# Kernel optimization log

Hardware: AMD Instinct MI355X
Metric: run time of the kernel (lower is better)

## Reference

```python
import jax, jax.numpy as jnp
import numpy as np

N = 100000      # nodes
E = 1600000     # directed edges (avg degree 16)
D_IN = 64
D_OUT = 64


def setup_inputs() -> dict:
    key = jax.random.key(0)
    k1, k2, k3, k4, k5 = jax.random.split(key, 5)
    x = jax.random.normal(k1, (N, D_IN), dtype=jnp.float32)
    edge_index = jax.random.randint(k2, (2, E), 0, N, dtype=jnp.int32)
    s_in = 1.0 / np.sqrt(D_IN)
    W_conv = jax.random.normal(k3, (D_IN, D_OUT), dtype=jnp.float32) * s_in
    b_conv = jnp.zeros((D_OUT,), dtype=jnp.float32)
    W_self = jax.random.normal(k4, (D_IN, D_OUT), dtype=jnp.float32) * s_in
    b_self = jax.random.normal(k5, (D_OUT,), dtype=jnp.float32) * s_in
    return {"x": x, "edge_index": edge_index, "W_conv": W_conv, "b_conv": b_conv,
            "W_self": W_self, "b_self": b_self, "n1": 400, "n2": 250}


def reference(x, edge_index, W_conv, b_conv, W_self, b_self, n1, n2):
    # GCNConv (PyG defaults): add self-loops, symmetric normalization,
    # out_i = sum_j norm_ij * (x_j @ W_conv) + b_conv; then self-loop linear + residual.
    n = x.shape[0]
    loops = jnp.arange(n, dtype=edge_index.dtype)
    row = jnp.concatenate([edge_index[0], loops])  # source nodes [E+N]
    col = jnp.concatenate([edge_index[1], loops])  # target nodes [E+N]
    deg = jax.ops.segment_sum(jnp.ones_like(col, dtype=x.dtype), col, num_segments=n)
    dinv = jnp.where(deg > 0, jax.lax.rsqrt(deg), 0.0)      # deg^{-1/2}
    norm = dinv[row] * dinv[col]                            # [E+N]
    xw = x @ W_conv                                         # [N, D_OUT]
    msg = xw[row] * norm[:, None]                           # gather + scale [E+N, D_OUT]
    x_neigh = jax.ops.segment_sum(msg, col, num_segments=n) + b_conv
    x_self = x @ W_self + b_self
    return x_self + x_neigh
```

## Files before the change

kernel.cpp:

```cpp
#include <hip/hip_runtime.h>

#define CAP 64
#define CHUNK 8192
#define NBINS_MAX 1024
#define CAPB 2560

typedef __attribute__((ext_vector_type(8))) short bf16x8;
typedef __attribute__((ext_vector_type(4))) float f32x4;

__device__ __forceinline__ unsigned short f2bf_rne(float f) {
    unsigned u = __builtin_bit_cast(unsigned, f);
    u += 0x7FFFu + ((u >> 16) & 1u);
    return (unsigned short)(u >> 16);
}
__device__ __forceinline__ float bf2f(unsigned short h) {
    return __builtin_bit_cast(float, (unsigned)h << 16);
}


__global__ void k_zero(int* __restrict__ gcur, int nbins, int* __restrict__ degovf,
                       int n, int* __restrict__ ovfc) {
    int i = blockIdx.x * blockDim.x + threadIdx.x;
    if (i < nbins) gcur[i] = 0;
    if (i < n) degovf[i] = 0;
    if (i == 0) *ovfc = 0;
}

__global__ void k_wprep(const float* __restrict__ Wc, const float* __restrict__ Ws,
                        unsigned short* __restrict__ bfrag) {
    const int t = threadIdx.x;
    for (int s = t; s < 2048; s += 256) {
        int lane = s & 63;
        int ct   = (s >> 6) & 3;
        int ks   = (s >> 8) & 1;
        int half = (s >> 9) & 1;
        int mat  = (s >> 10) & 1;
        const float* W = mat ? Ws : Wc;
        int d = ct * 16 + (lane & 15);
        int kbase = ks * 32 + (lane >> 4) * 8;
#pragma unroll
        for (int j = 0; j < 8; ++j) {
            float v = W[(kbase + j) * 64 + d];
            unsigned u = __builtin_bit_cast(unsigned, v);
            unsigned short hi = (unsigned short)(u >> 16);
            unsigned short elem;
            if (half == 0) {
                elem = hi;
            } else {
                float fh = __builtin_bit_cast(float, (unsigned)hi << 16);
                float fl = v - fh;
                elem = (unsigned short)(__builtin_bit_cast(unsigned, fl) >> 16);
            }
            bfrag[(size_t)s * 8 + j] = elem;
        }
    }
}

__global__ __launch_bounds__(512) void k_bin(
    const int* __restrict__ row, const int* __restrict__ col, int e, int nbins,
    int* __restrict__ gcur, unsigned int* __restrict__ records,
    int* __restrict__ degovf, int* __restrict__ ovf, int* __restrict__ ovfc)
{
    __shared__ int hist[NBINS_MAX];
    __shared__ int lofs[NBINS_MAX];
    __shared__ int gadj[NBINS_MAX];
    __shared__ int tscan[512];
    __shared__ unsigned int stage[CHUNK];
    __shared__ unsigned short sbin[CHUNK];

    const int t = threadIdx.x;
    const int base = blockIdx.x * CHUNK;
    int cnt = e - base; if (cnt > CHUNK) cnt = CHUNK;
    if (cnt <= 0) return;

    for (int i = t; i < nbins; i += 512) hist[i] = 0;
    __syncthreads();

    for (int k = t; k < cnt; k += 512) atomicAdd(&hist[col[base + k] >> 7], 1);
    __syncthreads();

    const int b0 = t * 2;
    int h0 = (b0 < nbins) ? hist[b0] : 0;
    int h1 = (b0 + 1 < nbins) ? hist[b0 + 1] : 0;
    int s = h0 + h1;
    tscan[t] = s;
    __syncthreads();
    for (int off = 1; off < 512; off <<= 1) {
        int v = (t >= off) ? tscan[t - off] : 0;
        __syncthreads();
        tscan[t] += v;
        __syncthreads();
    }
    const int tbase = tscan[t] - s;

    if (b0 < nbins) {
        int gb = h0 ? atomicAdd(&gcur[b0], h0) : 0;
        lofs[b0] = tbase; gadj[b0] = gb - tbase;
    }
    if (b0 + 1 < nbins) {
        int lb = tbase + h0;
        int gb = h1 ? atomicAdd(&gcur[b0 + 1], h1) : 0;
        lofs[b0 + 1] = lb; gadj[b0 + 1] = gb - lb;
    }
    __syncthreads();

    for (int k = t; k < cnt; k += 512) {
        int c = col[base + k];
        int r = row[base + k];
        int b = c >> 7;
        int slot = atomicAdd(&lofs[b], 1);
        stage[slot] = ((unsigned)r << 7) | (unsigned)(c & 127);
        sbin[slot] = (unsigned short)b;
    }
    __syncthreads();

    for (int k = t; k < cnt; k += 512) {
        unsigned rec = stage[k];
        int b = sbin[k];
        int g = gadj[b] + k;
        if (g < CAPB) {
            records[(size_t)b * CAPB + g] = rec;
        } else {
            int q = atomicAdd(ovfc, 1);
            int c = (b << 7) | (int)(rec & 127u);
            ovf[2 * q]     = (int)(rec >> 7);
            ovf[2 * q + 1] = c;
            atomicAdd(&degovf[c], 1);
        }
    }
}

__global__ __launch_bounds__(256) void k_dinv(
    const int* __restrict__ gcur, const unsigned int* __restrict__ records,
    const int* __restrict__ degovf, float* __restrict__ dinv, int n)
{
    __shared__ int lh[128];
    const int b = blockIdx.x, t = threadIdx.x;
    if (t < 128) lh[t] = 0;
    __syncthreads();
    int m = gcur[b]; if (m > CAPB) m = CAPB;
    const unsigned int* rb = records + (size_t)b * CAPB;
    for (int k = t; k < m; k += 256) atomicAdd(&lh[rb[k] & 127u], 1);
    __syncthreads();
    if (t < 128) {
        int node = (b << 7) + t;
        if (node < n) dinv[node] = rsqrtf((float)(lh[t] + degovf[node] + 1));
    }
}

__global__ __launch_bounds__(256) void k_gemm5(
    const float* __restrict__ x, const unsigned short* __restrict__ bfrag,
    const float* __restrict__ bc, const float* __restrict__ bs,
    const float* __restrict__ dinv, unsigned short* __restrict__ ybf,
    float* __restrict__ out, int n)
{
    const int t = threadIdx.x;
    const int lane = t & 63;
    const int wid = t >> 6;
    const int rt0 = blockIdx.x * 128 + wid * 32;
    if (rt0 >= n) return;

    const int arow = lane & 15;
    const int kgrp = lane >> 4;

    bf16x8 a_hi[2][2], a_lo[2][2];
#pragma unroll
    for (int rt = 0; rt < 2; ++rt) {
        int row = rt0 + rt * 16 + arow;
        if (row >= n) row = n - 1;
        const float* xp = x + (size_t)row * 64 + kgrp * 8;
#pragma unroll
        for (int ks = 0; ks < 2; ++ks) {
            float4 f0 = *(const float4*)(xp + ks * 32);
            float4 f1 = *(const float4*)(xp + ks * 32 + 4);
            float f[8] = {f0.x, f0.y, f0.z, f0.w, f1.x, f1.y, f1.z, f1.w};
            bf16x8 h, l;
#pragma unroll
            for (int j = 0; j < 8; ++j) {
                unsigned u = __builtin_bit_cast(unsigned, f[j]);
                unsigned short hj = (unsigned short)(u >> 16);
                float fh = __builtin_bit_cast(float, (unsigned)hj << 16);
                float fl = f[j] - fh;
                unsigned short lj = (unsigned short)(__builtin_bit_cast(unsigned, fl) >> 16);
                h[j] = (short)hj;
                l[j] = (short)lj;
            }
            a_hi[rt][ks] = h;
            a_lo[rt][ks] = l;
        }
    }

    f32x4 acc[2][2][4];
#pragma unroll
    for (int m = 0; m < 2; ++m)
#pragma unroll
        for (int rt = 0; rt < 2; ++rt)
#pragma unroll
            for (int ct = 0; ct < 4; ++ct)
                acc[m][rt][ct] = (f32x4){0.f, 0.f, 0.f, 0.f};

#pragma unroll
    for (int mat = 0; mat < 2; ++mat) {
#pragma unroll
        for (int ks = 0; ks < 2; ++ks) {
#pragma unroll
            for (int ct = 0; ct < 4; ++ct) {
                const bf16x8 bh = *(const bf16x8*)(bfrag + ((size_t)((((mat * 2 + 0) * 2 + ks) * 4 + ct) * 64 + lane)) * 8);
                const bf16x8 bl = *(const bf16x8*)(bfrag + ((size_t)((((mat * 2 + 1) * 2 + ks) * 4 + ct) * 64 + lane)) * 8);
#pragma unroll
                for (int rt = 0; rt < 2; ++rt) {
                    acc[mat][rt][ct] = __builtin_amdgcn_mfma_f32_16x16x32_bf16(a_hi[rt][ks], bh, acc[mat][rt][ct], 0, 0, 0);
                    acc[mat][rt][ct] = __builtin_amdgcn_mfma_f32_16x16x32_bf16(a_lo[rt][ks], bh, acc[mat][rt][ct], 0, 0, 0);
                    acc[mat][rt][ct] = __builtin_amdgcn_mfma_f32_16x16x32_bf16(a_hi[rt][ks], bl, acc[mat][rt][ct], 0, 0, 0);
                }
            }
        }
    }

    const int dcol = lane & 15;
    const int rbase = (lane >> 4) * 4;
    float di[2][4];
#pragma unroll
    for (int rt = 0; rt < 2; ++rt)
#pragma unroll
        for (int reg = 0; reg < 4; ++reg) {
            int row = rt0 + rt * 16 + rbase + reg;
            di[rt][reg] = dinv[(row < n) ? row : (n - 1)];
        }

#pragma unroll
    for (int ct = 0; ct < 4; ++ct) {
        int d = ct * 16 + dcol;
        float bias = bc[d] + bs[d];
#pragma unroll
        for (int rt = 0; rt < 2; ++rt) {
#pragma unroll
            for (int reg = 0; reg < 4; ++reg) {
                int row = rt0 + rt * 16 + rbase + reg;
                if (row < n) {
                    float dv = di[rt][reg];
                    float zc = acc[0][rt][ct][reg];
                    ybf[(size_t)row * 64 + d] = f2bf_rne(zc * dv);
                    out[(size_t)row * 64 + d] = acc[1][rt][ct][reg] + bias + dv * dv * zc;
                }
            }
        }
    }
}

__global__ __launch_bounds__(512) void k_gather_bin2(
    const int* __restrict__ gcur, const unsigned int* __restrict__ records,
    const unsigned short* __restrict__ ybf, const float* __restrict__ dinv,
    float* __restrict__ out, int n)
{
    __shared__ unsigned int srec[CAPB];
    __shared__ int slist[CAPB];
    __shared__ int scnt[128];
    __shared__ int sinc[128];
    __shared__ int scur[128];

    const int b = blockIdx.x, t = threadIdx.x;
    int m = gcur[b]; if (m > CAPB) m = CAPB;

    if (t < 128) scnt[t] = 0;
    __syncthreads();

    for (int k = t; k < m; k += 512) {
        unsigned r = __builtin_nontemporal_load(&records[(size_t)b * CAPB + k]);
        srec[k] = r;
        atomicAdd(&scnt[r & 127u], 1);
    }
    __syncthreads();

    if (t < 128) sinc[t] = scnt[t];
    __syncthreads();
    for (int off = 1; off < 128; off <<= 1) {
        int v = 0;
        if (t < 128 && t >= off) v = sinc[t - off];
        __syncthreads();
        if (t < 128) sinc[t] += v;
        __syncthreads();
    }
    if (t < 128) scur[t] = sinc[t] - scnt[t];
    __syncthreads();

    for (int k = t; k < m; k += 512) {
        unsigned r = srec[k];
        int slot = atomicAdd(&scur[r & 127u], 1);
        slist[slot] = (int)(r >> 7);
    }
    __syncthreads();

    const int wave = t >> 6, lane = t & 63;
    for (int i = wave; i < 128; i += 8) {
        int node = (b << 7) + i;
        if (node >= n) break;
        int cnt = scnt[i];
        if (cnt == 0) continue;
        int beg = sinc[i] - cnt;
        float acc = 0.f;
        for (int base = 0; base < cnt; base += 64) {
            int mm = cnt - base; if (mm > 64) mm = 64;
            int rl = (lane < mm) ? slist[beg + base + lane] : 0;
            float a0=0.f,a1=0.f,a2=0.f,a3=0.f,a4=0.f,a5=0.f,a6=0.f,a7=0.f;
            int k = 0;
            for (; k + 8 <= mm; k += 8) {
                int r0=__shfl(rl,k+0), r1=__shfl(rl,k+1), r2=__shfl(rl,k+2), r3=__shfl(rl,k+3);
                int r4=__shfl(rl,k+4), r5=__shfl(rl,k+5), r6=__shfl(rl,k+6), r7=__shfl(rl,k+7);
                unsigned short v0 = ybf[(size_t)r0*64 + lane];
                unsigned short v1 = ybf[(size_t)r1*64 + lane];
                unsigned short v2 = ybf[(size_t)r2*64 + lane];
                unsigned short v3 = ybf[(size_t)r3*64 + lane];
                unsigned short v4 = ybf[(size_t)r4*64 + lane];
                unsigned short v5 = ybf[(size_t)r5*64 + lane];
                unsigned short v6 = ybf[(size_t)r6*64 + lane];
                unsigned short v7 = ybf[(size_t)r7*64 + lane];
                a0 += bf2f(v0); a1 += bf2f(v1); a2 += bf2f(v2); a3 += bf2f(v3);
                a4 += bf2f(v4); a5 += bf2f(v5); a6 += bf2f(v6); a7 += bf2f(v7);
            }
            for (; k + 2 <= mm; k += 2) {
                int r0=__shfl(rl,k+0), r1=__shfl(rl,k+1);
                a0 += bf2f(ybf[(size_t)r0*64 + lane]);
                a1 += bf2f(ybf[(size_t)r1*64 + lane]);
            }
            if (k < mm) { int r0=__shfl(rl,k); a0 += bf2f(ybf[(size_t)r0*64 + lane]); }
            acc += ((a0+a1)+(a2+a3)) + ((a4+a5)+(a6+a7));
        }
        float* op = out + (size_t)node*64 + lane;
        float prev = __builtin_nontemporal_load(op);
        __builtin_nontemporal_store(prev + dinv[node] * acc, op);
    }
}

__global__ void k_ovf2(const int* __restrict__ ovfc, const int* __restrict__ ovf,
                       const float* __restrict__ dinv, const unsigned short* __restrict__ ybf,
                       float* __restrict__ out) {
    int m = *ovfc;
    long long total = (long long)m * 64;
    for (long long idx = blockIdx.x * blockDim.x + threadIdx.x; idx < total;
         idx += (long long)gridDim.x * blockDim.x) {
        int q = (int)(idx >> 6);
        int j = (int)(idx & 63);
        int r = ovf[2 * q], c = ovf[2 * q + 1];
        float s = dinv[c];
        float v = bf2f(ybf[(size_t)r * 64 + j]);
        unsafeAtomicAdd(out + (size_t)c * 64 + j, s * v);
    }
}


__global__ void k_init(int* __restrict__ cnt, int* __restrict__ ovf_cnt, int n) {
    int i = blockIdx.x * blockDim.x + threadIdx.x;
    if (i < n) cnt[i] = 0;
    if (i == 0) *ovf_cnt = 0;
}

__global__ void k_fill_pad(const int* __restrict__ row, const int* __restrict__ col,
                           int* __restrict__ cnt, int* __restrict__ bucket,
                           int* __restrict__ ovf, int* __restrict__ ovf_cnt, int e) {
    int i = blockIdx.x * blockDim.x + threadIdx.x;
    if (i >= e) return;
    int c = col[i];
    int p = atomicAdd(&cnt[c], 1);
    if (p < CAP) bucket[(size_t)c * CAP + p] = row[i];
    else { int q = atomicAdd(ovf_cnt, 1); ovf[q] = i; }
}

__global__ __launch_bounds__(256) void k_gemm(
    const float* __restrict__ x, const float* __restrict__ Wc,
    const float* __restrict__ bc, const float* __restrict__ Ws,
    const float* __restrict__ bs, const int* __restrict__ deg, int add,
    float* __restrict__ dinv, float* __restrict__ y,
    float* __restrict__ out, int n)
{
    __shared__ __align__(16) float sWc[64 * 64];
    __shared__ __align__(16) float sWs[64 * 64];
    __shared__ __align__(16) float sx[64 * 64];
    const int t = threadIdx.x;

    for (int i = t; i < 1024; i += 256) {
        ((float4*)sWc)[i] = ((const float4*)Wc)[i];
        ((float4*)sWs)[i] = ((const float4*)Ws)[i];
    }
    const int row0 = blockIdx.x * 64;
    int nrows = n - row0; if (nrows > 64) nrows = 64;
    for (int i = t; i < nrows * 16; i += 256) {
        ((float4*)sx)[i] = ((const float4*)(x + (size_t)row0 * 64))[i];
    }
    __syncthreads();

    const int d = t & 63;
    const int g = t >> 6;

    float wcr[64], wsr[64];
#pragma unroll
    for (int k = 0; k < 64; ++k) { wcr[k] = sWc[k * 64 + d]; wsr[k] = sWs[k * 64 + d]; }

    const float bcd = bc[d], bsd = bs[d];

    for (int rr = g * 16; rr < (g + 1) * 16; ++rr) {
        if (rr >= nrows) break;
        float accC = 0.f, accS = 0.f;
        const float4* xv4 = (const float4*)(sx + rr * 64);
#pragma unroll
        for (int q = 0; q < 16; ++q) {
            float4 xv = xv4[q];
            accC += xv.x*wcr[4*q+0] + xv.y*wcr[4*q+1] + xv.z*wcr[4*q+2] + xv.w*wcr[4*q+3];
            accS += xv.x*wsr[4*q+0] + xv.y*wsr[4*q+1] + xv.z*wsr[4*q+2] + xv.w*wsr[4*q+3];
        }
        const int r = row0 + rr;
        const float di = rsqrtf((float)(deg[r] + add));
        if (d == 0) dinv[r] = di;
        const float yv = accC * di;
        y[(size_t)r * 64 + d] = yv;
        out[(size_t)r * 64 + d] = accS + bsd + bcd + di * yv;
    }
}

__global__ __launch_bounds__(256) void k_gather_pad(
    const int* __restrict__ cnt, const int* __restrict__ bucket,
    const float* __restrict__ y, float* __restrict__ out, int n)
{
    const int node = blockIdx.x * 4 + (threadIdx.x >> 6);
    if (node >= n) return;
    const int lane = threadIdx.x & 63;
    int m = cnt[node];
    const float di = rsqrtf((float)(m + 1));
    if (m > CAP) m = CAP;
    if (m == 0) return;

    int rl = (lane < m) ? bucket[(size_t)node * CAP + lane] : 0;

    float a0=0.f,a1=0.f,a2=0.f,a3=0.f,a4=0.f,a5=0.f,a6=0.f,a7=0.f;
    int k = 0;
    for (; k + 8 <= m; k += 8) {
        int r0=__shfl(rl,k+0), r1=__shfl(rl,k+1), r2=__shfl(rl,k+2), r3=__shfl(rl,k+3);
        int r4=__shfl(rl,k+4), r5=__shfl(rl,k+5), r6=__shfl(rl,k+6), r7=__shfl(rl,k+7);
        a0 += y[(size_t)r0*64 + lane];
        a1 += y[(size_t)r1*64 + lane];
        a2 += y[(size_t)r2*64 + lane];
        a3 += y[(size_t)r3*64 + lane];
        a4 += y[(size_t)r4*64 + lane];
        a5 += y[(size_t)r5*64 + lane];
        a6 += y[(size_t)r6*64 + lane];
        a7 += y[(size_t)r7*64 + lane];
    }
    for (; k + 2 <= m; k += 2) {
        int r0=__shfl(rl,k+0), r1=__shfl(rl,k+1);
        a0 += y[(size_t)r0*64 + lane];
        a1 += y[(size_t)r1*64 + lane];
    }
    if (k < m) { int r0=__shfl(rl,k); a0 += y[(size_t)r0*64 + lane]; }

    float acc = ((a0+a1)+(a2+a3)) + ((a4+a5)+(a6+a7));
    out[(size_t)node*64 + lane] += di * acc;
}

__global__ void k_ovf_idx(const int* __restrict__ ovf_cnt, const int* __restrict__ ovf,
                          const int* __restrict__ row, const int* __restrict__ col,
                          const float* __restrict__ dinv, const float* __restrict__ y,
                          float* __restrict__ out) {
    int m = *ovf_cnt;
    long long total = (long long)m * 16;
    for (long long idx = blockIdx.x*blockDim.x+threadIdx.x; idx < total;
         idx += (long long)gridDim.x*blockDim.x) {
        int ei = ovf[idx >> 4];
        int j = (int)(idx & 15);
        int r = row[ei], c = col[ei];
        float s = dinv[c];
        float4 v = ((const float4*)y)[(size_t)r*16 + j];
        float* o = out + (size_t)c*64 + (j<<2);
        unsafeAtomicAdd(o+0, s*v.x);
        unsafeAtomicAdd(o+1, s*v.y);
        unsafeAtomicAdd(o+2, s*v.z);
        unsafeAtomicAdd(o+3, s*v.w);
    }
}

__global__ void k_deg_init(int* __restrict__ deg, int n) {
    int i = blockIdx.x * blockDim.x + threadIdx.x;
    if (i < n) deg[i] = 1;
}

__global__ void k_deg_count(const int* __restrict__ col, int* __restrict__ deg, int e) {
    int i = blockIdx.x * blockDim.x + threadIdx.x;
    if (i < e) atomicAdd(&deg[col[i]], 1);
}

__global__ __launch_bounds__(256) void k_scatter(
    const int* __restrict__ row, const int* __restrict__ col,
    const float* __restrict__ dinv, const float* __restrict__ y,
    float* __restrict__ out, int e)
{
    int idx = blockIdx.x * blockDim.x + threadIdx.x;
    int eidx = idx >> 4;
    if (eidx >= e) return;
    int j = idx & 15;
    int r = row[eidx];
    int c = col[eidx];
    float s = dinv[c];
    float4 v = ((const float4*)y)[(size_t)r * 16 + j];
    float* o = out + (size_t)c * 64 + (j << 2);
    unsafeAtomicAdd(o + 0, s * v.x);
    unsafeAtomicAdd(o + 1, s * v.y);
    unsafeAtomicAdd(o + 2, s * v.z);
    unsafeAtomicAdd(o + 3, s * v.w);
}

extern "C" void kernel_launch(void* const* d_in, const int* in_sizes, int n_in,
                              void* d_out, int out_size, void* d_ws, size_t ws_size,
                              hipStream_t stream) {
    const float* x  = (const float*)d_in[0];
    const int*   ei = (const int*)d_in[1];
    const float* Wc = (const float*)d_in[2];
    const float* bc = (const float*)d_in[3];
    const float* Ws = (const float*)d_in[4];
    const float* bs = (const float*)d_in[5];
    float* out = (float*)d_out;

    const int n = in_sizes[0] / 64;
    const int e = in_sizes[1] / 2;
    const int* rowi = ei;
    const int* coli = ei + e;

    auto align = [](size_t v) { return (v + 255) & ~(size_t)255; };
    char* ws = (char*)d_ws;
    const int nbins = (n + 127) >> 7;

    size_t m_dinv = 0;
    size_t m_y    = align(m_dinv + (size_t)n * 4);
    size_t m_gcur = align(m_y    + (size_t)n * 128);
    size_t m_rec  = align(m_gcur + (size_t)nbins * 4);
    size_t m_dov  = align(m_rec  + (size_t)nbins * CAPB * 4);
    size_t m_ovf  = align(m_dov  + (size_t)n * 4);
    size_t m_ovfc = align(m_ovf  + (size_t)e * 8);
    size_t m_bfr  = align(m_ovfc + 256);
    size_t m_tot  = m_bfr + 32768;

    size_t p_cnt  = 0;
    size_t p_dinv = align(p_cnt  + (size_t)n * 4);
    size_t p_y    = align(p_dinv + (size_t)n * 4);
    size_t p_bkt  = align(p_y    + (size_t)n * 256);
    size_t p_ovf  = align(p_bkt  + (size_t)n * CAP * 4);
    size_t p_ovfc = align(p_ovf  + (size_t)e * 4);
    size_t p_tot  = p_ovfc + 256;

    if (nbins <= NBINS_MAX && m_tot <= ws_size) {
        float* dinv = (float*)(ws + m_dinv);
        unsigned short* ybf = (unsigned short*)(ws + m_y);
        int*   gcur = (int*)(ws + m_gcur);
        unsigned int* rec = (unsigned int*)(ws + m_rec);
        int*   dov  = (int*)(ws + m_dov);
        int*   ovf  = (int*)(ws + m_ovf);
        int*   ovfc = (int*)(ws + m_ovfc);
        unsigned short* bfrag = (unsigned short*)(ws + m_bfr);

        int zmax = (n > nbins) ? n : nbins;
        k_zero<<<(zmax + 255) / 256, 256, 0, stream>>>(gcur, nbins, dov, n, ovfc);
        k_wprep<<<1, 256, 0, stream>>>(Wc, Ws, bfrag);
        k_bin<<<(e + CHUNK - 1) / CHUNK, 512, 0, stream>>>(rowi, coli, e, nbins,
                                                           gcur, rec, dov, ovf, ovfc);
        k_dinv<<<nbins, 256, 0, stream>>>(gcur, rec, dov, dinv, n);
        k_gemm5<<<(n + 127) / 128, 256, 0, stream>>>(x, bfrag, bc, bs, dinv, ybf, out, n);
        k_gather_bin2<<<nbins, 512, 0, stream>>>(gcur, rec, ybf, dinv, out, n);
        k_ovf2<<<64, 256, 0, stream>>>(ovfc, ovf, dinv, ybf, out);
    } else if (p_tot <= ws_size) {
        int*   cnt    = (int*)(ws + p_cnt);
        float* dinv   = (float*)(ws + p_dinv);
        float* y      = (float*)(ws + p_y);
        int*   bucket = (int*)(ws + p_bkt);
        int*   ovf    = (int*)(ws + p_ovf);
        int*   ovfc   = (int*)(ws + p_ovfc);

        k_init<<<(n + 255) / 256, 256, 0, stream>>>(cnt, ovfc, n);
        k_fill_pad<<<(e + 255) / 256, 256, 0, stream>>>(rowi, coli, cnt, bucket, ovf, ovfc, e);
        k_gemm<<<(n + 63) / 64, 256, 0, stream>>>(x, Wc, bc, Ws, bs, cnt, 1, dinv, y, out, n);
        k_gather_pad<<<(n + 3) / 4, 256, 0, stream>>>(cnt, bucket, y, out, n);
        k_ovf_idx<<<64, 256, 0, stream>>>(ovfc, ovf, rowi, coli, dinv, y, out);
    } else {
        size_t a_deg  = 0;
        size_t a_dinv = align(a_deg  + (size_t)n * 4);
        size_t a_y    = align(a_dinv + (size_t)n * 4);
        int*   deg  = (int*)(ws + a_deg);
        float* dinv = (float*)(ws + a_dinv);
        float* y    = (float*)(ws + a_y);
        k_deg_init<<<(n + 255) / 256, 256, 0, stream>>>(deg, n);
        k_deg_count<<<(e + 255) / 256, 256, 0, stream>>>(coli, deg, e);
        k_gemm<<<(n + 63) / 64, 256, 0, stream>>>(x, Wc, bc, Ws, bs, deg, 0, dinv, y, out, n);
        long long tot = (long long)e * 16;
        k_scatter<<<(int)((tot + 255) / 256), 256, 0, stream>>>(rowi, coli, dinv, y, out, e);
    }
}
```

Baseline: 115.1 us.

## Split gather bins across two blocks and fuse weight prep into zero kernel

The gather kernel now launches two blocks per 128-node bin. Each block handles 64 destination nodes and filters the bin's records to its own half, which doubles block-level parallelism at the cost of each block reading all records of the bin. The weight-fragment preparation is merged into the zeroing kernel as an extra last block, removing one kernel launch. The gather change trades redundant record loading and LDS work for more concurrent blocks (782 to 1564).

```diff
diff --git a/kernel.cpp b/kernel.cpp
--- a/kernel.cpp
+++ b/kernel.cpp
@@ -18,42 +18,43 @@
 }
 
 
-__global__ void k_zero(int* __restrict__ gcur, int nbins, int* __restrict__ degovf,
-                       int n, int* __restrict__ ovfc) {
-    int i = blockIdx.x * blockDim.x + threadIdx.x;
+__global__ void k_zero2(int* __restrict__ gcur, int nbins, int* __restrict__ degovf,
+                        int n, int* __restrict__ ovfc,
+                        const float* __restrict__ Wc, const float* __restrict__ Ws,
+                        unsigned short* __restrict__ bfrag) {
+    const int t = threadIdx.x;
+    if (blockIdx.x == gridDim.x - 1) {
+        for (int s = t; s < 2048; s += 256) {
+            int lane = s & 63;
+            int ct   = (s >> 6) & 3;
+            int ks   = (s >> 8) & 1;
+            int half = (s >> 9) & 1;
+            int mat  = (s >> 10) & 1;
+            const float* W = mat ? Ws : Wc;
+            int d = ct * 16 + (lane & 15);
+            int kbase = ks * 32 + (lane >> 4) * 8;
+#pragma unroll
+            for (int j = 0; j < 8; ++j) {
+                float v = W[(kbase + j) * 64 + d];
+                unsigned u = __builtin_bit_cast(unsigned, v);
+                unsigned short hi = (unsigned short)(u >> 16);
+                unsigned short elem;
+                if (half == 0) {
+                    elem = hi;
+                } else {
+                    float fh = __builtin_bit_cast(float, (unsigned)hi << 16);
+                    float fl = v - fh;
+                    elem = (unsigned short)(__builtin_bit_cast(unsigned, fl) >> 16);
+                }
+                bfrag[(size_t)s * 8 + j] = elem;
+            }
+        }
+        return;
+    }
+    int i = blockIdx.x * blockDim.x + t;
     if (i < nbins) gcur[i] = 0;
     if (i < n) degovf[i] = 0;
     if (i == 0) *ovfc = 0;
-}
-
-__global__ void k_wprep(const float* __restrict__ Wc, const float* __restrict__ Ws,
-                        unsigned short* __restrict__ bfrag) {
-    const int t = threadIdx.x;
-    for (int s = t; s < 2048; s += 256) {
-        int lane = s & 63;
-        int ct   = (s >> 6) & 3;
-        int ks   = (s >> 8) & 1;
-        int half = (s >> 9) & 1;
-        int mat  = (s >> 10) & 1;
-        const float* W = mat ? Ws : Wc;
-        int d = ct * 16 + (lane & 15);
-        int kbase = ks * 32 + (lane >> 4) * 8;
-#pragma unroll
-        for (int j = 0; j < 8; ++j) {
-            float v = W[(kbase + j) * 64 + d];
-            unsigned u = __builtin_bit_cast(unsigned, v);
-            unsigned short hi = (unsigned short)(u >> 16);
-            unsigned short elem;
-            if (half == 0) {
-                elem = hi;
-            } else {
-                float fh = __builtin_bit_cast(float, (unsigned)hi << 16);
-                float fl = v - fh;
-                elem = (unsigned short)(__builtin_bit_cast(unsigned, fl) >> 16);
-            }
-            bfrag[(size_t)s * 8 + j] = elem;
-        }
-    }
 }
 
 __global__ __launch_bounds__(512) void k_bin(
@@ -248,52 +249,59 @@
     }
 }
 
-__global__ __launch_bounds__(512) void k_gather_bin2(
+__global__ __launch_bounds__(512) void k_gather_bin2h(
     const int* __restrict__ gcur, const unsigned int* __restrict__ records,
     const unsigned short* __restrict__ ybf, const float* __restrict__ dinv,
     float* __restrict__ out, int n)
 {
     __shared__ unsigned int srec[CAPB];
     __shared__ int slist[CAPB];
-    __shared__ int scnt[128];
-    __shared__ int sinc[128];
-    __shared__ int scur[128];
-
-    const int b = blockIdx.x, t = threadIdx.x;
+    __shared__ int scnt[64];
+    __shared__ int sinc[64];
+    __shared__ int scur[64];
+
+    const int b = blockIdx.x >> 1;
+    const int half = blockIdx.x & 1;
+    const int nbase = (b << 7) + (half << 6);
+    const int t = threadIdx.x;
     int m = gcur[b]; if (m > CAPB) m = CAPB;
 
-    if (t < 128) scnt[t] = 0;
+    if (t < 64) scnt[t] = 0;
     __syncthreads();
 
     for (int k = t; k < m; k += 512) {
         unsigned r = __builtin_nontemporal_load(&records[(size_t)b * CAPB + k]);
         srec[k] = r;
-        atomicAdd(&scnt[r & 127u], 1);
-    }
-    __syncthreads();
-
-    if (t < 128) sinc[t] = scnt[t];
-    __syncthreads();
-    for (int off = 1; off < 128; off <<= 1) {
+        unsigned c = r & 127u;
+        if ((int)(c >> 6) == half) atomicAdd(&scnt[c & 63u], 1);
+    }
+    __syncthreads();
+
+    if (t < 64) sinc[t] = scnt[t];
+    __syncthreads();
+    for (int off = 1; off < 64; off <<= 1) {
         int v = 0;
-        if (t < 128 && t >= off) v = sinc[t - off];
+        if (t < 64 && t >= off) v = sinc[t - off];
         __syncthreads();
-        if (t < 128) sinc[t] += v;
+        if (t < 64) sinc[t] += v;
         __syncthreads();
     }
-    if (t < 128) scur[t] = sinc[t] - scnt[t];
+    if (t < 64) scur[t] = sinc[t] - scnt[t];
     __syncthreads();
 
     for (int k = t; k < m; k += 512) {
         unsigned r = srec[k];
-        int slot = atomicAdd(&scur[r & 127u], 1);
-        slist[slot] = (int)(r >> 7);
+        unsigned c = r & 127u;
+        if ((int)(c >> 6) == half) {
+            int slot = atomicAdd(&scur[c & 63u], 1);
+            slist[slot] = (int)(r >> 7);
+        }
     }
     __syncthreads();
 
     const int wave = t >> 6, lane = t & 63;
-    for (int i = wave; i < 128; i += 8) {
-        int node = (b << 7) + i;
+    for (int i = wave; i < 64; i += 8) {
+        int node = nbase + i;
         if (node >= n) break;
         int cnt = scnt[i];
         if (cnt == 0) continue;
@@ -556,13 +564,13 @@
         unsigned short* bfrag = (unsigned short*)(ws + m_bfr);
 
         int zmax = (n > nbins) ? n : nbins;
-        k_zero<<<(zmax + 255) / 256, 256, 0, stream>>>(gcur, nbins, dov, n, ovfc);
-        k_wprep<<<1, 256, 0, stream>>>(Wc, Ws, bfrag);
+        k_zero2<<<(zmax + 255) / 256 + 1, 256, 0, stream>>>(gcur, nbins, dov, n, ovfc,
+                                                            Wc, Ws, bfrag);
         k_bin<<<(e + CHUNK - 1) / CHUNK, 512, 0, stream>>>(rowi, coli, e, nbins,
                                                            gcur, rec, dov, ovf, ovfc);
         k_dinv<<<nbins, 256, 0, stream>>>(gcur, rec, dov, dinv, n);
         k_gemm5<<<(n + 127) / 128, 256, 0, stream>>>(x, bfrag, bc, bs, dinv, ybf, out, n);
-        k_gather_bin2<<<nbins, 512, 0, stream>>>(gcur, rec, ybf, dinv, out, n);
+        k_gather_bin2h<<<nbins * 2, 512, 0, stream>>>(gcur, rec, ybf, dinv, out, n);
         k_ovf2<<<64, 256, 0, stream>>>(ovfc, ovf, dinv, ybf, out);
     } else if (p_tot <= ws_size) {
         int*   cnt    = (int*)(ws + p_cnt);
```

Result: no change. 114.1 us (-0.9%).
